# Kernel optimization log

Hardware: AMD Instinct MI355X
Metric: run time of the kernel (lower is better)

## Reference

```python
import jax, jax.numpy as jnp
import numpy as np

TOP_K = 2


def setup_inputs() -> dict:
    key = jax.random.key(0)
    ks = jax.random.split(key, 6)
    B, S, D, F, E = 4, 2048, 1024, 4096, 8
    sd = 1.0 / np.sqrt(D)
    sf = 1.0 / np.sqrt(F)
    return {
        "x": jax.random.normal(ks[0], (B, S, D), dtype=jnp.float32),
        "gate_w": jax.random.normal(ks[1], (D, E), dtype=jnp.float32) * sd,
        "w1": jax.random.normal(ks[2], (E, D, F), dtype=jnp.float32) * sd,
        "b1": jax.random.normal(ks[3], (E, F), dtype=jnp.float32) * 0.01,
        "w2": jax.random.normal(ks[4], (E, F, D), dtype=jnp.float32) * sf,
        "b2": jax.random.normal(ks[5], (E, D), dtype=jnp.float32) * 0.01,
    }


def reference(x, gate_w, w1, b1, w2, b2):
    B, S, D = x.shape
    E = gate_w.shape[1]
    xf = x.reshape(-1, D)                        # [T, D], T = B*S
    T = xf.shape[0]

    # Gating: top-k logits, softmax over the selected k (in fp32, as in torch)
    logits = xf @ gate_w                         # [T, E]
    top_vals, top_idx = jax.lax.top_k(logits, TOP_K)            # [T, K]
    wts = jax.nn.softmax(top_vals.astype(jnp.float32), axis=-1).astype(x.dtype)

    # Dense combine weights: combine[t, e] = sum_k wts[t,k] * [top_idx[t,k]==e]
    rows = jnp.arange(T)[:, None]
    combine = jnp.zeros((T, E), dtype=x.dtype).at[rows, top_idx].add(wts)

    # Expert FFNs (dropout is identity in eval; torch GELU default = exact erf)
    out = jnp.zeros_like(xf)
    for e in range(E):
        h = jax.nn.gelu(xf @ w1[e] + b1[e], approximate=False)  # [T, F]
        out = out + combine[:, e:e + 1] * (h @ w2[e] + b2[e])
    return out.reshape(B, S, D)
```

## Files before the change

### kernel.cpp

```cpp
#include <hip/hip_runtime.h>


#define T_TOK 8192
#define D_DIM 1024
#define F_DIM 4096
#define E_NUM 8
#define BM 128
#define BN 128
#define BK 32
#define NK1 (D_DIM / BK)
#define NK2 (F_DIM / BK)
#define MAX_TILES (T_TOK * 2 / BM + E_NUM)

typedef float f32x4 __attribute__((ext_vector_type(4)));
typedef short bf16x8 __attribute__((ext_vector_type(8)));

__device__ __forceinline__ unsigned short f2bf(float f) {
  union { float f; unsigned u; } v; v.f = f;
  unsigned r = v.u + 0x7FFFu + ((v.u >> 16) & 1u);
  return (unsigned short)(r >> 16);
}

__device__ __forceinline__ void async_cp16(const unsigned short* g, unsigned short* l) {
  __builtin_amdgcn_global_load_lds((__attribute__((address_space(1))) void*)g,
                                   (__attribute__((address_space(3))) void*)l,
                                   16, 0, 0);
}

#define WAIT_VM4 asm volatile("s_waitcnt vmcnt(4)" ::: "memory")
#define WAIT_LGKM0 asm volatile("s_waitcnt lgkmcnt(0)" ::: "memory")
#define RAW_BARRIER asm volatile("s_barrier" ::: "memory")


__global__ void cast_x_kernel(const float* __restrict__ src,
                              unsigned short* __restrict__ dst, int n4) {
  int i = blockIdx.x * blockDim.x + threadIdx.x;
  if (i >= n4) return;
  float4 v = ((const float4*)src)[i];
  ushort4 o;
  o.x = f2bf(v.x); o.y = f2bf(v.y); o.z = f2bf(v.z); o.w = f2bf(v.w);
  ((ushort4*)dst)[i] = o;
}

__global__ __launch_bounds__(256) void transpose_cast_kernel(
    const float* __restrict__ src, unsigned short* __restrict__ dst,
    int R, int C) {
  __shared__ float tile[64][68];
  int e = blockIdx.z;
  src += (size_t)e * R * C;
  dst += (size_t)e * R * C;
  int c0 = blockIdx.x * 64;
  int r0 = blockIdx.y * 64;
  int t = threadIdx.x;
  int cl = (t & 15) * 4, rl = t >> 4;
#pragma unroll
  for (int i = 0; i < 4; ++i) {
    int r = rl + i * 16;
    float4 v = *(const float4*)(src + (size_t)(r0 + r) * C + c0 + cl);
    *(float4*)&tile[r][cl] = v;
  }
  __syncthreads();
  int rl2 = (t & 15) * 4, cl2 = t >> 4;
#pragma unroll
  for (int i = 0; i < 4; ++i) {
    int c = cl2 + i * 16;
    ushort4 o;
    o.x = f2bf(tile[rl2 + 0][c]);
    o.y = f2bf(tile[rl2 + 1][c]);
    o.z = f2bf(tile[rl2 + 2][c]);
    o.w = f2bf(tile[rl2 + 3][c]);
    *(ushort4*)(dst + (size_t)(c0 + c) * R + r0 + rl2) = o;
  }
}

__global__ __launch_bounds__(256) void gate_kernel(
    const float* __restrict__ x, const float* __restrict__ gw,
    float* __restrict__ topk_w, int* __restrict__ topk_e) {
  int t = (blockIdx.x * 256 + threadIdx.x) >> 6;
  int lane = threadIdx.x & 63;
  const float* xr = x + (size_t)t * D_DIM;
  float acc[8];
#pragma unroll
  for (int e = 0; e < 8; ++e) acc[e] = 0.f;
  for (int j = 0; j < D_DIM / 64; ++j) {
    int d = lane + 64 * j;
    float xv = xr[d];
    float4 g0 = ((const float4*)(gw + (size_t)d * 8))[0];
    float4 g1 = ((const float4*)(gw + (size_t)d * 8))[1];
    acc[0] += xv * g0.x; acc[1] += xv * g0.y;
    acc[2] += xv * g0.z; acc[3] += xv * g0.w;
    acc[4] += xv * g1.x; acc[5] += xv * g1.y;
    acc[6] += xv * g1.z; acc[7] += xv * g1.w;
  }
#pragma unroll
  for (int off = 32; off > 0; off >>= 1) {
#pragma unroll
    for (int e = 0; e < 8; ++e) acc[e] += __shfl_xor(acc[e], off);
  }
  if (lane == 0) {
    int e0 = 0; float v0 = acc[0];
#pragma unroll
    for (int e = 1; e < 8; ++e)
      if (acc[e] > v0) { v0 = acc[e]; e0 = e; }
    int e1 = -1; float v1 = -1e30f;
#pragma unroll
    for (int e = 0; e < 8; ++e)
      if (e != e0 && acc[e] > v1) { v1 = acc[e]; e1 = e; }
    float ex = expf(v1 - v0);
    float inv = 1.f / (1.f + ex);
    topk_w[2 * t] = inv;
    topk_w[2 * t + 1] = ex * inv;
    topk_e[2 * t] = e0;
    topk_e[2 * t + 1] = e1;
  }
}

__global__ void scatter_kernel(const int* __restrict__ topk_e,
                               int* __restrict__ cnt, int* __restrict__ assign) {
  int idx = blockIdx.x * blockDim.x + threadIdx.x;
  int e = topk_e[idx];
  int pos = atomicAdd(&cnt[e], 1);
  assign[e * T_TOK + pos] = idx;
}

__global__ void tiles_kernel(const int* __restrict__ cnt,
                             int* __restrict__ ndesc, int4* __restrict__ desc) {
  if (threadIdx.x != 0) return;
  int nt = 0, hb = 0;
  for (int e = 0; e < E_NUM; ++e) {
    int c = cnt[e];
    for (int s = 0; s < c; s += BM) {
      int4 d;
      d.x = e; d.y = s; d.z = hb;
      d.w = (c - s < BM) ? (c - s) : BM;
      desc[nt++] = d;
    }
    hb += c;
  }
  *ndesc = nt;
}


__global__ __launch_bounds__(256) void gemm1_kernel(
    const unsigned short* __restrict__ xb, const unsigned short* __restrict__ w1t,
    const float* __restrict__ b1, const int* __restrict__ assign,
    const int* __restrict__ ndesc, const int4* __restrict__ desc,
    unsigned short* __restrict__ H) {
  int tileid = blockIdx.y;
  if (tileid >= *ndesc) return;
  int4 dc = desc[tileid];
  int e = dc.x, start = dc.y, hbase = dc.z, mcnt = dc.w;
  int n0 = blockIdx.x * BN;

  __shared__ __attribute__((aligned(16))) unsigned short As[2][BM * BK];
  __shared__ __attribute__((aligned(16))) unsigned short Bs[2][BN * BK];

  int tid = threadIdx.x, lane = tid & 63, wv = tid >> 6;

  const unsigned short* gA[2]; const unsigned short* gB[2];
  int loff[2];
#pragma unroll
  for (int s = 0; s < 2; ++s) {
    int L = tid + s * 256;
    int row = L >> 2, cc = L & 3;
    int g = (cc - row) & 3;
    int rowc = row < mcnt ? row : (mcnt - 1);
    int a = assign[e * T_TOK + start + rowc];
    gA[s] = xb + (size_t)(a >> 1) * D_DIM + g * 8;
    gB[s] = w1t + (size_t)(e * F_DIM + n0 + row) * D_DIM + g * 8;
    loff[s] = (s * 256 + wv * 64) * 8;
  }

  int kc16 = lane >> 4, r16 = lane & 15;
  int m_off = (wv & 1) * 64, n_off = (wv >> 1) * 64;
  int aoff[4], boff[4];
#pragma unroll
  for (int i = 0; i < 4; ++i) {
    int ra = m_off + i * 16 + r16;
    aoff[i] = ra * 32 + ((kc16 + ra) & 3) * 8;
    int rb = n_off + i * 16 + r16;
    boff[i] = rb * 32 + ((kc16 + rb) & 3) * 8;
  }

  f32x4 acc[4][4];
#pragma unroll
  for (int i = 0; i < 4; ++i)
#pragma unroll
    for (int j = 0; j < 4; ++j) acc[i][j] = (f32x4){0.f, 0.f, 0.f, 0.f};

  auto issue = [&](int t, int b) {
    int kc = (t < NK1 ? t : NK1 - 1) * BK;
#pragma unroll
    for (int s = 0; s < 2; ++s) {
      async_cp16(gA[s] + kc, &As[b][loff[s]]);
      async_cp16(gB[s] + kc, &Bs[b][loff[s]]);
    }
  };
  auto step = [&](int kt, int b) {
    WAIT_VM4;
    RAW_BARRIER;
    bf16x8 af[4], bfr[4];
#pragma unroll
    for (int i = 0; i < 4; ++i) af[i] = *(const bf16x8*)(&As[b][0] + aoff[i]);
#pragma unroll
    for (int i = 0; i < 4; ++i) bfr[i] = *(const bf16x8*)(&Bs[b][0] + boff[i]);
    WAIT_LGKM0;
    RAW_BARRIER;
    issue(kt + 2, b);
#pragma unroll
    for (int i = 0; i < 4; ++i)
#pragma unroll
      for (int j = 0; j < 4; ++j)
        acc[i][j] = __builtin_amdgcn_mfma_f32_16x16x32_bf16(af[i], bfr[j], acc[i][j], 0, 0, 0);
  };

  issue(0, 0);
  issue(1, 1);
  for (int kt = 0; kt < NK1; kt += 2) { step(kt, 0); step(kt + 1, 1); }

  int col = lane & 15, rbase = (lane >> 4) * 4;
  float bias[4];
#pragma unroll
  for (int j = 0; j < 4; ++j) bias[j] = b1[e * F_DIM + n0 + n_off + j * 16 + col];
#pragma unroll
  for (int i = 0; i < 4; ++i) {
#pragma unroll
    for (int rg = 0; rg < 4; ++rg) {
      int r = m_off + i * 16 + rbase + rg;
      if (r < mcnt) {
        unsigned short* hrow = H + (size_t)(hbase + start + r) * F_DIM + n0 + n_off + col;
#pragma unroll
        for (int j = 0; j < 4; ++j) {
          float v = acc[i][j][rg] + bias[j];
          v = 0.5f * v * (1.0f + erff(v * 0.70710678118654752f));
          hrow[j * 16] = f2bf(v);
        }
      }
    }
  }
}

__global__ __launch_bounds__(256) void gemm2_kernel(
    const unsigned short* __restrict__ H, const unsigned short* __restrict__ w2t,
    const float* __restrict__ b2, const int* __restrict__ assign,
    const float* __restrict__ topk_w,
    const int* __restrict__ ndesc, const int4* __restrict__ desc,
    float* __restrict__ out) {
  int tileid = blockIdx.y;
  if (tileid >= *ndesc) return;
  int4 dc = desc[tileid];
  int e = dc.x, start = dc.y, hbase = dc.z, mcnt = dc.w;
  int n0 = blockIdx.x * BN;

  __shared__ __attribute__((aligned(16))) unsigned short As[2][BM * BK];
  __shared__ __attribute__((aligned(16))) unsigned short Bs[2][BN * BK];

  int tid = threadIdx.x, lane = tid & 63, wv = tid >> 6;

  const unsigned short* gA[2]; const unsigned short* gB[2];
  int loff[2];
#pragma unroll
  for (int s = 0; s < 2; ++s) {
    int L = tid + s * 256;
    int row = L >> 2, cc = L & 3;
    int g = (cc - row) & 3;
    int rowc = row < mcnt ? row : (mcnt - 1);
    gA[s] = H + (size_t)(hbase + start + rowc) * F_DIM + g * 8;
    gB[s] = w2t + (size_t)(e * D_DIM + n0 + row) * F_DIM + g * 8;
    loff[s] = (s * 256 + wv * 64) * 8;
  }

  int kc16 = lane >> 4, r16 = lane & 15;
  int m_off = (wv & 1) * 64, n_off = (wv >> 1) * 64;
  int aoff[4], boff[4];
#pragma unroll
  for (int i = 0; i < 4; ++i) {
    int ra = m_off + i * 16 + r16;
    aoff[i] = ra * 32 + ((kc16 + ra) & 3) * 8;
    int rb = n_off + i * 16 + r16;
    boff[i] = rb * 32 + ((kc16 + rb) & 3) * 8;
  }

  f32x4 acc[4][4];
#pragma unroll
  for (int i = 0; i < 4; ++i)
#pragma unroll
    for (int j = 0; j < 4; ++j) acc[i][j] = (f32x4){0.f, 0.f, 0.f, 0.f};

  auto issue = [&](int t, int b) {
    int kc = (t < NK2 ? t : NK2 - 1) * BK;
#pragma unroll
    for (int s = 0; s < 2; ++s) {
      async_cp16(gA[s] + kc, &As[b][loff[s]]);
      async_cp16(gB[s] + kc, &Bs[b][loff[s]]);
    }
  };
  auto step = [&](int kt, int b) {
    WAIT_VM4;
    RAW_BARRIER;
    bf16x8 af[4], bfr[4];
#pragma unroll
    for (int i = 0; i < 4; ++i) af[i] = *(const bf16x8*)(&As[b][0] + aoff[i]);
#pragma unroll
    for (int i = 0; i < 4; ++i) bfr[i] = *(const bf16x8*)(&Bs[b][0] + boff[i]);
    WAIT_LGKM0;
    RAW_BARRIER;
    issue(kt + 2, b);
#pragma unroll
    for (int i = 0; i < 4; ++i)
#pragma unroll
      for (int j = 0; j < 4; ++j)
        acc[i][j] = __builtin_amdgcn_mfma_f32_16x16x32_bf16(af[i], bfr[j], acc[i][j], 0, 0, 0);
  };

  issue(0, 0);
  issue(1, 1);
  for (int kt = 0; kt < NK2; kt += 2) { step(kt, 0); step(kt + 1, 1); }

  int col = lane & 15, rbase = (lane >> 4) * 4;
  float bias[4];
#pragma unroll
  for (int j = 0; j < 4; ++j) bias[j] = b2[e * D_DIM + n0 + n_off + j * 16 + col];
#pragma unroll
  for (int i = 0; i < 4; ++i) {
#pragma unroll
    for (int rg = 0; rg < 4; ++rg) {
      int r = m_off + i * 16 + rbase + rg;
      if (r < mcnt) {
        int a = assign[e * T_TOK + start + r];
        float wt = topk_w[a];
        float* orow = out + (size_t)(a >> 1) * D_DIM + n0 + n_off + col;
#pragma unroll
        for (int j = 0; j < 4; ++j) {
          float v = acc[i][j][rg] + bias[j];
          atomicAdd(orow + j * 16, wt * v);
        }
      }
    }
  }
}


extern "C" void kernel_launch(void* const* d_in, const int* in_sizes, int n_in,
                              void* d_out, int out_size, void* d_ws, size_t ws_size,
                              hipStream_t stream) {
  const float* x      = (const float*)d_in[0];
  const float* gate_w = (const float*)d_in[1];
  const float* w1     = (const float*)d_in[2];
  const float* b1     = (const float*)d_in[3];
  const float* w2     = (const float*)d_in[4];
  const float* b2     = (const float*)d_in[5];
  float* out = (float*)d_out;

  char* ws = (char*)d_ws;
  size_t off = 0;
  auto alloc = [&](size_t bytes) {
    char* p = ws + off;
    off = (off + bytes + 255) & ~(size_t)255;
    return p;
  };
  unsigned short* xb   = (unsigned short*)alloc((size_t)T_TOK * D_DIM * 2);
  unsigned short* w1t  = (unsigned short*)alloc((size_t)E_NUM * D_DIM * F_DIM * 2);
  unsigned short* w2t  = (unsigned short*)alloc((size_t)E_NUM * D_DIM * F_DIM * 2);
  unsigned short* Hbuf = (unsigned short*)alloc((size_t)2 * T_TOK * F_DIM * 2);
  float* topk_w = (float*)alloc((size_t)2 * T_TOK * 4);
  int* topk_e   = (int*)alloc((size_t)2 * T_TOK * 4);
  int* assign   = (int*)alloc((size_t)E_NUM * T_TOK * 4);
  int* cnt      = (int*)alloc(64);
  int* ndesc    = (int*)alloc(64);
  int4* desc    = (int4*)alloc((size_t)MAX_TILES * 16);

  hipMemsetAsync(cnt, 0, 64, stream);
  hipMemsetAsync(out, 0, (size_t)out_size * 4, stream);

  cast_x_kernel<<<(T_TOK * D_DIM / 4 + 255) / 256, 256, 0, stream>>>(
      x, xb, T_TOK * D_DIM / 4);
  transpose_cast_kernel<<<dim3(F_DIM / 64, D_DIM / 64, E_NUM), 256, 0, stream>>>(
      w1, w1t, D_DIM, F_DIM);
  transpose_cast_kernel<<<dim3(D_DIM / 64, F_DIM / 64, E_NUM), 256, 0, stream>>>(
      w2, w2t, F_DIM, D_DIM);
  gate_kernel<<<T_TOK / 4, 256, 0, stream>>>(x, gate_w, topk_w, topk_e);
  scatter_kernel<<<2 * T_TOK / 256, 256, 0, stream>>>(topk_e, cnt, assign);
  tiles_kernel<<<1, 64, 0, stream>>>(cnt, ndesc, desc);
  gemm1_kernel<<<dim3(F_DIM / BN, MAX_TILES), 256, 0, stream>>>(
      xb, w1t, b1, assign, ndesc, desc, Hbuf);
  gemm2_kernel<<<dim3(D_DIM / BN, MAX_TILES), 256, 0, stream>>>(
      Hbuf, w2t, b2, assign, topk_w, ndesc, desc, out);
}
```

Baseline: 918.7 us.

## Use 512-thread blocks with 8 waves per 128x128 GEMM tile

Both expert GEMM kernels now launch 8 waves per block instead of 4, each wave computing a 64x32 sub-tile with half the accumulators, and each thread issuing one async copy per operand per K step. The aim is more resident waves to hide global and LDS latency. In exchange, LDS fragment reads per MFMA rise and more waves hit each barrier. The transpose kernel also switches to a 65-wide padded LDS tile with scalar stores to reduce bank conflicts.

```diff
diff --git a/kernel.cpp b/kernel.cpp
--- a/kernel.cpp
+++ b/kernel.cpp
@@ -27,7 +27,7 @@
                                    16, 0, 0);
 }
 
-#define WAIT_VM4 asm volatile("s_waitcnt vmcnt(4)" ::: "memory")
+#define WAIT_VM2 asm volatile("s_waitcnt vmcnt(2)" ::: "memory")
 #define WAIT_LGKM0 asm volatile("s_waitcnt lgkmcnt(0)" ::: "memory")
 #define RAW_BARRIER asm volatile("s_barrier" ::: "memory")
 
@@ -45,7 +45,7 @@
 __global__ __launch_bounds__(256) void transpose_cast_kernel(
     const float* __restrict__ src, unsigned short* __restrict__ dst,
     int R, int C) {
-  __shared__ float tile[64][68];
+  __shared__ float tile[64][65];
   int e = blockIdx.z;
   src += (size_t)e * R * C;
   dst += (size_t)e * R * C;
@@ -57,7 +57,10 @@
   for (int i = 0; i < 4; ++i) {
     int r = rl + i * 16;
     float4 v = *(const float4*)(src + (size_t)(r0 + r) * C + c0 + cl);
-    *(float4*)&tile[r][cl] = v;
+    tile[r][cl + 0] = v.x;
+    tile[r][cl + 1] = v.y;
+    tile[r][cl + 2] = v.z;
+    tile[r][cl + 3] = v.w;
   }
   __syncthreads();
   int rl2 = (t & 15) * 4, cl2 = t >> 4;
@@ -141,7 +144,7 @@
 }
 
 
-__global__ __launch_bounds__(256) void gemm1_kernel(
+__global__ __launch_bounds__(512, 6) void gemm1_kernel(
     const unsigned short* __restrict__ xb, const unsigned short* __restrict__ w1t,
     const float* __restrict__ b1, const int* __restrict__ assign,
     const int* __restrict__ ndesc, const int4* __restrict__ desc,
@@ -157,60 +160,54 @@
 
   int tid = threadIdx.x, lane = tid & 63, wv = tid >> 6;
 
-  const unsigned short* gA[2]; const unsigned short* gB[2];
-  int loff[2];
-#pragma unroll
-  for (int s = 0; s < 2; ++s) {
-    int L = tid + s * 256;
-    int row = L >> 2, cc = L & 3;
-    int g = (cc - row) & 3;
-    int rowc = row < mcnt ? row : (mcnt - 1);
-    int a = assign[e * T_TOK + start + rowc];
-    gA[s] = xb + (size_t)(a >> 1) * D_DIM + g * 8;
-    gB[s] = w1t + (size_t)(e * F_DIM + n0 + row) * D_DIM + g * 8;
-    loff[s] = (s * 256 + wv * 64) * 8;
-  }
+  int row = tid >> 2, cc = tid & 3;
+  int g = (cc - row) & 3;
+  int rowc = row < mcnt ? row : (mcnt - 1);
+  int a0 = assign[e * T_TOK + start + rowc];
+  const unsigned short* gA = xb + (size_t)(a0 >> 1) * D_DIM + g * 8;
+  const unsigned short* gB = w1t + (size_t)(e * F_DIM + n0 + row) * D_DIM + g * 8;
+  int loff = wv * 512;
 
   int kc16 = lane >> 4, r16 = lane & 15;
-  int m_off = (wv & 1) * 64, n_off = (wv >> 1) * 64;
-  int aoff[4], boff[4];
+  int m_off = (wv & 1) * 64, n_off = (wv >> 1) * 32;
+  int aoff[4], boff[2];
 #pragma unroll
   for (int i = 0; i < 4; ++i) {
     int ra = m_off + i * 16 + r16;
     aoff[i] = ra * 32 + ((kc16 + ra) & 3) * 8;
-    int rb = n_off + i * 16 + r16;
-    boff[i] = rb * 32 + ((kc16 + rb) & 3) * 8;
-  }
-
-  f32x4 acc[4][4];
+  }
+#pragma unroll
+  for (int j = 0; j < 2; ++j) {
+    int rb = n_off + j * 16 + r16;
+    boff[j] = rb * 32 + ((kc16 + rb) & 3) * 8;
+  }
+
+  f32x4 acc[4][2];
 #pragma unroll
   for (int i = 0; i < 4; ++i)
 #pragma unroll
-    for (int j = 0; j < 4; ++j) acc[i][j] = (f32x4){0.f, 0.f, 0.f, 0.f};
+    for (int j = 0; j < 2; ++j) acc[i][j] = (f32x4){0.f, 0.f, 0.f, 0.f};
 
   auto issue = [&](int t, int b) {
     int kc = (t < NK1 ? t : NK1 - 1) * BK;
-#pragma unroll
-    for (int s = 0; s < 2; ++s) {
-      async_cp16(gA[s] + kc, &As[b][loff[s]]);
-      async_cp16(gB[s] + kc, &Bs[b][loff[s]]);
-    }
+    async_cp16(gA + kc, &As[b][loff]);
+    async_cp16(gB + kc, &Bs[b][loff]);
   };
   auto step = [&](int kt, int b) {
-    WAIT_VM4;
+    WAIT_VM2;
     RAW_BARRIER;
-    bf16x8 af[4], bfr[4];
+    bf16x8 af[4], bfr[2];
 #pragma unroll
     for (int i = 0; i < 4; ++i) af[i] = *(const bf16x8*)(&As[b][0] + aoff[i]);
 #pragma unroll
-    for (int i = 0; i < 4; ++i) bfr[i] = *(const bf16x8*)(&Bs[b][0] + boff[i]);
+    for (int j = 0; j < 2; ++j) bfr[j] = *(const bf16x8*)(&Bs[b][0] + boff[j]);
     WAIT_LGKM0;
     RAW_BARRIER;
     issue(kt + 2, b);
 #pragma unroll
     for (int i = 0; i < 4; ++i)
 #pragma unroll
-      for (int j = 0; j < 4; ++j)
+      for (int j = 0; j < 2; ++j)
         acc[i][j] = __builtin_amdgcn_mfma_f32_16x16x32_bf16(af[i], bfr[j], acc[i][j], 0, 0, 0);
   };
 
@@ -219,9 +216,9 @@
   for (int kt = 0; kt < NK1; kt += 2) { step(kt, 0); step(kt + 1, 1); }
 
   int col = lane & 15, rbase = (lane >> 4) * 4;
-  float bias[4];
-#pragma unroll
-  for (int j = 0; j < 4; ++j) bias[j] = b1[e * F_DIM + n0 + n_off + j * 16 + col];
+  float bias[2];
+#pragma unroll
+  for (int j = 0; j < 2; ++j) bias[j] = b1[e * F_DIM + n0 + n_off + j * 16 + col];
 #pragma unroll
   for (int i = 0; i < 4; ++i) {
 #pragma unroll
@@ -230,7 +227,7 @@
       if (r < mcnt) {
         unsigned short* hrow = H + (size_t)(hbase + start + r) * F_DIM + n0 + n_off + col;
 #pragma unroll
-        for (int j = 0; j < 4; ++j) {
+        for (int j = 0; j < 2; ++j) {
           float v = acc[i][j][rg] + bias[j];
           v = 0.5f * v * (1.0f + erff(v * 0.70710678118654752f));
           hrow[j * 16] = f2bf(v);
@@ -240,7 +237,7 @@
   }
 }
 
-__global__ __launch_bounds__(256) void gemm2_kernel(
+__global__ __launch_bounds__(512, 6) void gemm2_kernel(
     const unsigned short* __restrict__ H, const unsigned short* __restrict__ w2t,
     const float* __restrict__ b2, const int* __restrict__ assign,
     const float* __restrict__ topk_w,
@@ -257,59 +254,53 @@
 
   int tid = threadIdx.x, lane = tid & 63, wv = tid >> 6;
 
-  const unsigned short* gA[2]; const unsigned short* gB[2];
-  int loff[2];
-#pragma unroll
-  for (int s = 0; s < 2; ++s) {
-    int L = tid + s * 256;
-    int row = L >> 2, cc = L & 3;
-    int g = (cc - row) & 3;
-    int rowc = row < mcnt ? row : (mcnt - 1);
-    gA[s] = H + (size_t)(hbase + start + rowc) * F_DIM + g * 8;
-    gB[s] = w2t + (size_t)(e * D_DIM + n0 + row) * F_DIM + g * 8;
-    loff[s] = (s * 256 + wv * 64) * 8;
-  }
+  int row = tid >> 2, cc = tid & 3;
+  int g = (cc - row) & 3;
+  int rowc = row < mcnt ? row : (mcnt - 1);
+  const unsigned short* gA = H + (size_t)(hbase + start + rowc) * F_DIM + g * 8;
+  const unsigned short* gB = w2t + (size_t)(e * D_DIM + n0 + row) * F_DIM + g * 8;
+  int loff = wv * 512;
 
   int kc16 = lane >> 4, r16 = lane & 15;
-  int m_off = (wv & 1) * 64, n_off = (wv >> 1) * 64;
-  int aoff[4], boff[4];
+  int m_off = (wv & 1) * 64, n_off = (wv >> 1) * 32;
+  int aoff[4], boff[2];
 #pragma unroll
   for (int i = 0; i < 4; ++i) {
     int ra = m_off + i * 16 + r16;
     aoff[i] = ra * 32 + ((kc16 + ra) & 3) * 8;
-    int rb = n_off + i * 16 + r16;
-    boff[i] = rb * 32 + ((kc16 + rb) & 3) * 8;
-  }
-
-  f32x4 acc[4][4];
+  }
+#pragma unroll
+  for (int j = 0; j < 2; ++j) {
+    int rb = n_off + j * 16 + r16;
+    boff[j] = rb * 32 + ((kc16 + rb) & 3) * 8;
+  }
+
+  f32x4 acc[4][2];
 #pragma unroll
   for (int i = 0; i < 4; ++i)
 #pragma unroll
-    for (int j = 0; j < 4; ++j) acc[i][j] = (f32x4){0.f, 0.f, 0.f, 0.f};
+    for (int j = 0; j < 2; ++j) acc[i][j] = (f32x4){0.f, 0.f, 0.f, 0.f};
 
   auto issue = [&](int t, int b) {
     int kc = (t < NK2 ? t : NK2 - 1) * BK;
-#pragma unroll
-    for (int s = 0; s < 2; ++s) {
-      async_cp16(gA[s] + kc, &As[b][loff[s]]);
-      async_cp16(gB[s] + kc, &Bs[b][loff[s]]);
-    }
+    async_cp16(gA + kc, &As[b][loff]);
+    async_cp16(gB + kc, &Bs[b][loff]);
   };
   auto step = [&](int kt, int b) {
-    WAIT_VM4;
+    WAIT_VM2;
     RAW_BARRIER;
-    bf16x8 af[4], bfr[4];
+    bf16x8 af[4], bfr[2];
 #pragma unroll
     for (int i = 0; i < 4; ++i) af[i] = *(const bf16x8*)(&As[b][0] + aoff[i]);
 #pragma unroll
-    for (int i = 0; i < 4; ++i) bfr[i] = *(const bf16x8*)(&Bs[b][0] + boff[i]);
+    for (int j = 0; j < 2; ++j) bfr[j] = *(const bf16x8*)(&Bs[b][0] + boff[j]);
     WAIT_LGKM0;
     RAW_BARRIER;
     issue(kt + 2, b);
 #pragma unroll
     for (int i = 0; i < 4; ++i)
 #pragma unroll
-      for (int j = 0; j < 4; ++j)
+      for (int j = 0; j < 2; ++j)
         acc[i][j] = __builtin_amdgcn_mfma_f32_16x16x32_bf16(af[i], bfr[j], acc[i][j], 0, 0, 0);
   };
 
@@ -318,9 +309,9 @@
   for (int kt = 0; kt < NK2; kt += 2) { step(kt, 0); step(kt + 1, 1); }
 
   int col = lane & 15, rbase = (lane >> 4) * 4;
-  float bias[4];
-#pragma unroll
-  for (int j = 0; j < 4; ++j) bias[j] = b2[e * D_DIM + n0 + n_off + j * 16 + col];
+  float bias[2];
+#pragma unroll
+  for (int j = 0; j < 2; ++j) bias[j] = b2[e * D_DIM + n0 + n_off + j * 16 + col];
 #pragma unroll
   for (int i = 0; i < 4; ++i) {
 #pragma unroll
@@ -331,7 +322,7 @@
         float wt = topk_w[a];
         float* orow = out + (size_t)(a >> 1) * D_DIM + n0 + n_off + col;
 #pragma unroll
-        for (int j = 0; j < 4; ++j) {
+        for (int j = 0; j < 2; ++j) {
           float v = acc[i][j][rg] + bias[j];
           atomicAdd(orow + j * 16, wt * v);
         }
@@ -382,8 +373,8 @@
   gate_kernel<<<T_TOK / 4, 256, 0, stream>>>(x, gate_w, topk_w, topk_e);
   scatter_kernel<<<2 * T_TOK / 256, 256, 0, stream>>>(topk_e, cnt, assign);
   tiles_kernel<<<1, 64, 0, stream>>>(cnt, ndesc, desc);
-  gemm1_kernel<<<dim3(F_DIM / BN, MAX_TILES), 256, 0, stream>>>(
+  gemm1_kernel<<<dim3(F_DIM / BN, MAX_TILES), 512, 0, stream>>>(
       xb, w1t, b1, assign, ndesc, desc, Hbuf);
-  gemm2_kernel<<<dim3(D_DIM / BN, MAX_TILES), 256, 0, stream>>>(
+  gemm2_kernel<<<dim3(D_DIM / BN, MAX_TILES), 512, 0, stream>>>(
       Hbuf, w2t, b2, assign, topk_w, ndesc, desc, out);
 }
```

After: 893.2 us. 1.03x faster.
